# Performance work log

Measured on AMD Instinct MI355X. Metric: run time of the kernel, lower is better.

## Reference

```python
import jax, jax.numpy as jnp
import numpy as np

N = 8192
NFEAT = 512
NHID = 512
NCLASS = 64
NLAYERS = 8
LAMDA = 0.5
ALPHA = 0.1
EDGE_P = 0.002  # ~16 avg degree


def setup_inputs() -> dict:
    key = jax.random.key(0)
    ks = jax.random.split(key, 6)
    x = jax.random.normal(ks[0], (N, NFEAT), dtype=jnp.float32)
    # sparse 0/1 adjacency, densified (the original densifies adj each layer)
    adj = (jax.random.uniform(ks[1], (N, N)) < EDGE_P).astype(jnp.float32)
    stdv1 = 1.0 / np.sqrt(NHID)
    fc1_W = jax.random.normal(ks[2], (NFEAT, NHID), dtype=jnp.float32) * stdv1
    fc1_b = jnp.zeros((NHID,), dtype=jnp.float32)
    # GraphConvolution.reset_parameters: uniform(-1/sqrt(out), 1/sqrt(out))
    conv_Ws = jax.random.uniform(ks[3], (NLAYERS, NHID, NHID), minval=-stdv1, maxval=stdv1, dtype=jnp.float32)
    stdv2 = 1.0 / np.sqrt(NCLASS)
    fc2_W = jax.random.normal(ks[4], (NHID, NCLASS), dtype=jnp.float32) * stdv2
    fc2_b = jnp.zeros((NCLASS,), dtype=jnp.float32)
    return {"x": x, "adj": adj, "fc1_W": fc1_W, "fc1_b": fc1_b,
            "conv_Ws": conv_Ws, "fc2_W": fc2_W, "fc2_b": fc2_b}


def reference(x, adj, fc1_W, fc1_b, conv_Ws, fc2_W, fc2_b):
    n = adj.shape[0]
    # A_hat = A + I ; P = D^{-1/2} A_hat D^{-1/2}  (diag matmuls -> row/col scaling)
    A_hat = adj + jnp.eye(n, dtype=adj.dtype)
    dinv = 1.0 / jnp.sqrt(jnp.sum(A_hat, axis=0))  # [N]
    P = dinv[:, None] * A_hat * dinv[None, :]      # identical every layer; compute once

    H0 = jax.nn.relu(x @ fc1_W + fc1_b)            # fc1 (dropout is identity: training=False)
    H = H0
    for i in range(NLAYERS):
        beta = float(np.log(LAMDA / (i + 1) + 1.0))
        init_res = (1.0 - ALPHA) * (P @ H) + ALPHA * H0
        # init_res @ ((1-beta) I + beta W) expanded:
        H = jax.nn.relu((1.0 - beta) * init_res + beta * (init_res @ conv_Ws[i]))
    logits = H @ fc2_W + fc2_b
    return -jax.nn.log_softmax(logits, axis=1)
```

## Files before the change

kernel.cpp:

```cpp
#include <hip/hip_runtime.h>
#include <hip/hip_bf16.h>
#include <cmath>

#define N_NODES 8192
#define NFEAT 512
#define NHID 512
#define NCLASS 64
#define NLAYERS 8
#define CAP 96

typedef __attribute__((ext_vector_type(8))) short bf16x8;
typedef __attribute__((ext_vector_type(4))) float f32x4;
typedef unsigned short u16;

__device__ inline float bf2f(short u) {
  union { unsigned int i; float f; } x;
  x.i = ((unsigned int)(u16)u) << 16;
  return x.f;
}
__device__ inline short f2bf(float f) {
  union { float f; unsigned int i; } x;
  x.f = f;
  unsigned int r = x.i + 0x7FFFu + ((x.i >> 16) & 1u);
  return (short)(r >> 16);
}

__global__ __launch_bounds__(256)
void extract_kernel(const float* __restrict__ adj, int* __restrict__ idx,
                    int* __restrict__ cnt, int* __restrict__ colcnt)
{
  __shared__ int s_cnt;
  const int i = blockIdx.x;
  if (threadIdx.x == 0) s_cnt = 0;
  __syncthreads();
  const uint4* row = (const uint4*)(adj + (size_t)i * N_NODES);
  for (int c = threadIdx.x; c < N_NODES / 4; c += 256) {
    uint4 v = row[c];
    if ((v.x | v.y | v.z | v.w) == 0u) continue;
    unsigned int vals[4] = {v.x, v.y, v.z, v.w};
    #pragma unroll
    for (int e = 0; e < 4; ++e) {
      if (vals[e] != 0u) {
        int p = atomicAdd(&s_cnt, 1);
        if (p < CAP) idx[(size_t)i * CAP + p] = c * 4 + e;
        atomicAdd(&colcnt[c * 4 + e], 1);
      }
    }
  }
  __syncthreads();
  if (threadIdx.x == 0) cnt[i] = min(s_cnt, CAP);
}

__global__ __launch_bounds__(256)
void dinv_kernel(const int* __restrict__ colcnt, float* __restrict__ dinv)
{
  int j = blockIdx.x * 256 + threadIdx.x;
  if (j < N_NODES) dinv[j] = 1.0f / sqrtf((float)colcnt[j] + 1.0f);
}

__global__ __launch_bounds__(256)
void cvt_bf16_kernel(const float* __restrict__ src, u16* __restrict__ dst, int n4)
{
  int i = blockIdx.x * 256 + threadIdx.x;
  if (i >= n4) return;
  float4 v = ((const float4*)src)[i];
  ushort4 o;
  o.x = (u16)f2bf(v.x); o.y = (u16)f2bf(v.y);
  o.z = (u16)f2bf(v.z); o.w = (u16)f2bf(v.w);
  ((ushort4*)dst)[i] = o;
}

__global__ __launch_bounds__(256)
void transpose_cast_kernel(const float* __restrict__ fc1W, const float* __restrict__ convW,
                           u16* __restrict__ Wt)
{
  __shared__ float tile[32][33];
  const int m = blockIdx.z;
  const float* src = (m == 0) ? fc1W : convW + (size_t)(m - 1) * NHID * NHID;
  u16* dst = Wt + (size_t)m * NHID * NHID;
  const int k0 = blockIdx.x * 32, n0 = blockIdx.y * 32;
  const int tx = threadIdx.x & 31, ty = threadIdx.x >> 5;
  #pragma unroll
  for (int r = 0; r < 32; r += 8)
    tile[ty + r][tx] = src[(size_t)(k0 + ty + r) * NHID + n0 + tx];
  __syncthreads();
  #pragma unroll
  for (int r = 0; r < 32; r += 8)
    dst[(size_t)(n0 + ty + r) * NHID + k0 + tx] = (u16)f2bf(tile[tx][ty + r]);
}

#define AS1 __attribute__((address_space(1)))
#define AS3 __attribute__((address_space(3)))

__device__ inline void load16(const void* g, void* l) {
  __builtin_amdgcn_global_load_lds((const AS1 void*)g, (AS3 void*)l, 16, 0, 0);
}

template<int MODE>
__global__ __launch_bounds__(256, 2)
void gemm_kernel(const u16* __restrict__ A, const u16* __restrict__ Bt,
                 const float* __restrict__ bias, const u16* __restrict__ skip,
                 const float* __restrict__ dinv, float cA, float cB,
                 u16* __restrict__ out0, u16* __restrict__ out1)
{
  constexpr int K = 512, N = 512;
  __shared__ u16 ldsA[2][64 * 32];
  __shared__ u16 ldsB[2][128 * 32];
  const int tid = threadIdx.x;
  const int wave = tid >> 6, lane = tid & 63;
  const int m0 = blockIdx.x * 64, n0 = blockIdx.y * 128;
  const int wr = wave >> 1, wc = wave & 1;
  const int lrow = lane & 15, lk = lane >> 4;

  f32x4 acc[2][4];
  #pragma unroll
  for (int a = 0; a < 2; ++a)
    #pragma unroll
    for (int b = 0; b < 4; ++b)
      acc[a][b] = (f32x4){0.f, 0.f, 0.f, 0.f};

  auto stage = [&](int b, int ks) {
    {
      const int c = wave * 64 + lane;
      load16(A + (size_t)(m0 + (c >> 2)) * K + ks + (c & 3) * 8,
             &ldsA[b][(wave * 64) * 8]);
    }
    #pragma unroll
    for (int r = 0; r < 2; ++r) {
      const int c = r * 256 + wave * 64 + lane;
      load16(Bt + (size_t)(n0 + (c >> 2)) * K + ks + (c & 3) * 8,
             &ldsB[b][(r * 256 + wave * 64) * 8]);
    }
  };

  stage(0, 0);
  __syncthreads();

  for (int t = 0; t < 16; ++t) {
    const int b = t & 1;
    if (t + 1 < 16) stage(b ^ 1, (t + 1) * 32);
    bf16x8 af[2], bfr[4];
    #pragma unroll
    for (int mi = 0; mi < 2; ++mi)
      af[mi] = *(const bf16x8*)&ldsA[b][(wr * 32 + mi * 16 + lrow) * 32 + lk * 8];
    #pragma unroll
    for (int ni = 0; ni < 4; ++ni)
      bfr[ni] = *(const bf16x8*)&ldsB[b][(wc * 64 + ni * 16 + lrow) * 32 + lk * 8];
    #pragma unroll
    for (int mi = 0; mi < 2; ++mi)
      #pragma unroll
      for (int ni = 0; ni < 4; ++ni)
        acc[mi][ni] = __builtin_amdgcn_mfma_f32_16x16x32_bf16(af[mi], bfr[ni], acc[mi][ni], 0, 0, 0);
    __syncthreads();
  }

  #pragma unroll
  for (int mi = 0; mi < 2; ++mi) {
    #pragma unroll
    for (int ni = 0; ni < 4; ++ni) {
      #pragma unroll
      for (int r = 0; r < 4; ++r) {
        const int row = m0 + wr * 32 + mi * 16 + lk * 4 + r;
        const int col = n0 + wc * 64 + ni * 16 + lrow;
        const size_t o = (size_t)row * N + col;
        float v = acc[mi][ni][r];
        if (MODE == 0) {
          v = fmaxf(v + bias[col], 0.f);
          out0[o] = (u16)f2bf(v);
          out1[o] = (u16)f2bf(dinv[row] * v);
        } else {
          v = fmaxf(cA * bf2f((short)skip[o]) + cB * v, 0.f);
          out0[o] = (u16)f2bf(MODE == 1 ? dinv[row] * v : v);
        }
      }
    }
  }
}

__global__ __launch_bounds__(256)
void spmm_kernel(const u16* __restrict__ Hs, const u16* __restrict__ H0,
                 const float* __restrict__ dinv, const int* __restrict__ idx,
                 const int* __restrict__ cnt, u16* __restrict__ IR)
{
  const int wave = threadIdx.x >> 6, lane = threadIdx.x & 63;
  const int i = blockIdx.x * 4 + wave;
  const int c0 = lane * 8;
  const int n = cnt[i];
  int jreg = 0;
  if (lane < n) jreg = idx[(size_t)i * CAP + lane] & (N_NODES - 1);

  float acc[8];
  #pragma unroll
  for (int e = 0; e < 8; ++e) acc[e] = 0.f;

  const int nn = min(n, 64);
  int t = 0;
  for (; t + 8 <= nn; t += 8) {
    bf16x8 v[8];
    #pragma unroll
    for (int u = 0; u < 8; ++u) {
      const int j = __shfl(jreg, t + u);
      v[u] = *(const bf16x8*)&Hs[(size_t)j * NHID + c0];
    }
    #pragma unroll
    for (int u = 0; u < 8; ++u)
      #pragma unroll
      for (int e = 0; e < 8; ++e)
        acc[e] += bf2f(v[u][e]);
  }
  for (; t < nn; ++t) {
    const int j = __shfl(jreg, t);
    bf16x8 v = *(const bf16x8*)&Hs[(size_t)j * NHID + c0];
    #pragma unroll
    for (int e = 0; e < 8; ++e) acc[e] += bf2f(v[e]);
  }
  for (; t < n; ++t) {
    const int j = idx[(size_t)i * CAP + t] & (N_NODES - 1);
    bf16x8 v = *(const bf16x8*)&Hs[(size_t)j * NHID + c0];
    #pragma unroll
    for (int e = 0; e < 8; ++e) acc[e] += bf2f(v[e]);
  }

  const float di = dinv[i];
  bf16x8 self = *(const bf16x8*)&Hs[(size_t)i * NHID + c0];
  bf16x8 h0   = *(const bf16x8*)&H0[(size_t)i * NHID + c0];
  bf16x8 ov;
  #pragma unroll
  for (int e = 0; e < 8; ++e) {
    float v = 0.9f * di * (acc[e] + bf2f(self[e])) + 0.1f * bf2f(h0[e]);
    ov[e] = f2bf(v);
  }
  *(bf16x8*)&IR[(size_t)i * NHID + c0] = ov;
}

__global__ __launch_bounds__(256)
void fc2_softmax_kernel(const u16* __restrict__ H, const float* __restrict__ W,
                        const float* __restrict__ b, float* __restrict__ out)
{
  __shared__ float sh[4][4][512];
  const int wave = threadIdx.x >> 6, lane = threadIdx.x & 63;
  const int rowBase = blockIdx.x * 16 + wave * 4;
  #pragma unroll
  for (int rr = 0; rr < 4; ++rr) {
    bf16x8 hv = *(const bf16x8*)&H[(size_t)(rowBase + rr) * NHID + lane * 8];
    #pragma unroll
    for (int e = 0; e < 8; ++e) sh[wave][rr][lane * 8 + e] = bf2f(hv[e]);
  }
  __syncthreads();
  const float bb = b[lane];
  float a0 = bb, a1 = bb, a2 = bb, a3 = bb;
  #pragma unroll 8
  for (int k = 0; k < 512; ++k) {
    const float w = W[k * 64 + lane];
    a0 += sh[wave][0][k] * w;
    a1 += sh[wave][1][k] * w;
    a2 += sh[wave][2][k] * w;
    a3 += sh[wave][3][k] * w;
  }
  float accs[4] = {a0, a1, a2, a3};
  #pragma unroll
  for (int rr = 0; rr < 4; ++rr) {
    const float v = accs[rr];
    float mx = v;
    for (int off = 32; off > 0; off >>= 1) mx = fmaxf(mx, __shfl_xor(mx, off));
    float s = __expf(v - mx);
    for (int off = 32; off > 0; off >>= 1) s += __shfl_xor(s, off);
    out[(size_t)(rowBase + rr) * NCLASS + lane] = -(v - mx - logf(s));
  }
}

extern "C" void kernel_launch(void* const* d_in, const int* in_sizes, int n_in,
                              void* d_out, int out_size, void* d_ws, size_t ws_size,
                              hipStream_t stream)
{
  const float* x     = (const float*)d_in[0];
  const float* adj   = (const float*)d_in[1];
  const float* fc1W  = (const float*)d_in[2];
  const float* fc1b  = (const float*)d_in[3];
  const float* convW = (const float*)d_in[4];
  const float* fc2W  = (const float*)d_in[5];
  const float* fc2b  = (const float*)d_in[6];
  float* out = (float*)d_out;

  char* ws = (char*)d_ws;
  size_t off = 0;
  auto alloc = [&](size_t bytes) -> void* {
    void* p = ws + off;
    off = (off + bytes + 255) & ~(size_t)255;
    return p;
  };
  u16*   xb   = (u16*)alloc((size_t)N_NODES * NFEAT * 2);
  u16*   Wt   = (u16*)alloc((size_t)9 * NHID * NHID * 2);
  u16*   H0   = (u16*)alloc((size_t)N_NODES * NHID * 2);
  u16*   HsA  = (u16*)alloc((size_t)N_NODES * NHID * 2);
  u16*   HsB  = (u16*)alloc((size_t)N_NODES * NHID * 2);
  u16*   IR   = (u16*)alloc((size_t)N_NODES * NHID * 2);
  int*   idx  = (int*)alloc((size_t)N_NODES * CAP * 4);
  int*   cnt  = (int*)alloc((size_t)N_NODES * 4);
  int*   colc = (int*)alloc((size_t)N_NODES * 4);
  float* dinv = (float*)alloc((size_t)N_NODES * 4);

  hipMemsetAsync(colc, 0, N_NODES * 4, stream);
  extract_kernel<<<N_NODES, 256, 0, stream>>>(adj, idx, cnt, colc);
  dinv_kernel<<<N_NODES / 256, 256, 0, stream>>>(colc, dinv);
  cvt_bf16_kernel<<<(N_NODES * NFEAT / 4) / 256, 256, 0, stream>>>(x, xb, N_NODES * NFEAT / 4);
  transpose_cast_kernel<<<dim3(16, 16, 9), 256, 0, stream>>>(fc1W, convW, Wt);

  gemm_kernel<0><<<dim3(128, 4), 256, 0, stream>>>(xb, Wt, fc1b, nullptr, dinv, 0.f, 0.f, H0, HsA);

  const u16* Hin = HsA;
  for (int i = 0; i < NLAYERS; ++i) {
    const double beta = log(0.5 / (double)(i + 1) + 1.0);
    const float cA = (float)(1.0 - beta), cB = (float)beta;
    spmm_kernel<<<N_NODES / 4, 256, 0, stream>>>(Hin, H0, dinv, idx, cnt, IR);
    u16* Hout = (Hin == HsA) ? HsB : HsA;
    if (i < NLAYERS - 1)
      gemm_kernel<1><<<dim3(128, 4), 256, 0, stream>>>(
          IR, Wt + (size_t)(i + 1) * NHID * NHID, nullptr, IR, dinv, cA, cB, Hout, nullptr);
    else
      gemm_kernel<2><<<dim3(128, 4), 256, 0, stream>>>(
          IR, Wt + (size_t)(i + 1) * NHID * NHID, nullptr, IR, dinv, cA, cB, Hout, nullptr);
    Hin = Hout;
  }

  fc2_softmax_kernel<<<N_NODES / 16, 256, 0, stream>>>((const u16*)Hin, fc2W, fc2b, out);
}
```

Baseline: 361.8 us.

## Fuse all post-extract stages into one persistent kernel with grid barriers

Result: slower. 1.155 ms (+219.3%).

```diff
diff --git a/kernel.cpp b/kernel.cpp
--- a/kernel.cpp
+++ b/kernel.cpp
@@ -8,10 +8,13 @@
 #define NCLASS 64
 #define NLAYERS 8
 #define CAP 96
+#define NBLK 512
 
 typedef __attribute__((ext_vector_type(8))) short bf16x8;
 typedef __attribute__((ext_vector_type(4))) float f32x4;
 typedef unsigned short u16;
+
+struct Coefs { float cA[8]; float cB[8]; };
 
 __device__ inline float bf2f(short u) {
   union { unsigned int i; float f; } x;
@@ -51,42 +54,69 @@
   if (threadIdx.x == 0) cnt[i] = min(s_cnt, CAP);
 }
 
-__global__ __launch_bounds__(256)
-void dinv_kernel(const int* __restrict__ colcnt, float* __restrict__ dinv)
-{
-  int j = blockIdx.x * 256 + threadIdx.x;
-  if (j < N_NODES) dinv[j] = 1.0f / sqrtf((float)colcnt[j] + 1.0f);
-}
-
-__global__ __launch_bounds__(256)
-void cvt_bf16_kernel(const float* __restrict__ src, u16* __restrict__ dst, int n4)
-{
-  int i = blockIdx.x * 256 + threadIdx.x;
-  if (i >= n4) return;
-  float4 v = ((const float4*)src)[i];
-  ushort4 o;
-  o.x = (u16)f2bf(v.x); o.y = (u16)f2bf(v.y);
-  o.z = (u16)f2bf(v.z); o.w = (u16)f2bf(v.w);
-  ((ushort4*)dst)[i] = o;
-}
-
-__global__ __launch_bounds__(256)
-void transpose_cast_kernel(const float* __restrict__ fc1W, const float* __restrict__ convW,
-                           u16* __restrict__ Wt)
-{
-  __shared__ float tile[32][33];
-  const int m = blockIdx.z;
-  const float* src = (m == 0) ? fc1W : convW + (size_t)(m - 1) * NHID * NHID;
-  u16* dst = Wt + (size_t)m * NHID * NHID;
-  const int k0 = blockIdx.x * 32, n0 = blockIdx.y * 32;
+__device__ inline void gridbar(int* bar, int phase) {
+  __syncthreads();
+  if (threadIdx.x == 0) {
+    __hip_atomic_fetch_add(&bar[phase], 1, __ATOMIC_RELEASE, __HIP_MEMORY_SCOPE_AGENT);
+    while (__hip_atomic_load(&bar[phase], __ATOMIC_RELAXED, __HIP_MEMORY_SCOPE_AGENT) < NBLK)
+      __builtin_amdgcn_s_sleep(1);
+    __builtin_amdgcn_fence(__ATOMIC_ACQUIRE, "agent");
+  }
+  __syncthreads();
+}
+
+__device__ void p_dinv(const int* __restrict__ colc, float* __restrict__ dinv) {
+  if (blockIdx.x < N_NODES / 256) {
+    const int j = blockIdx.x * 256 + threadIdx.x;
+    dinv[j] = 1.0f / sqrtf((float)colc[j] + 1.0f);
+  }
+}
+
+__device__ void p_cvt(const float* __restrict__ x, u16* __restrict__ xb) {
+  const float4* src = (const float4*)x;
+  #pragma unroll
+  for (int it = 0; it < 8; ++it) {
+    const int i = it * (NBLK * 256) + blockIdx.x * 256 + threadIdx.x;
+    float4 v = src[i];
+    ushort4 o;
+    o.x = (u16)f2bf(v.x); o.y = (u16)f2bf(v.y);
+    o.z = (u16)f2bf(v.z); o.w = (u16)f2bf(v.w);
+    ((ushort4*)xb)[i] = o;
+  }
+}
+
+__device__ void p_transpose(const float* __restrict__ fc1W, const float* __restrict__ convW,
+                            u16* __restrict__ Wt, const Coefs& co, char* smem) {
+  float (*tile)[33] = (float(*)[33])smem;
   const int tx = threadIdx.x & 31, ty = threadIdx.x >> 5;
-  #pragma unroll
-  for (int r = 0; r < 32; r += 8)
-    tile[ty + r][tx] = src[(size_t)(k0 + ty + r) * NHID + n0 + tx];
-  __syncthreads();
-  #pragma unroll
-  for (int r = 0; r < 32; r += 8)
-    dst[(size_t)(n0 + ty + r) * NHID + k0 + tx] = (u16)f2bf(tile[tx][ty + r]);
+  for (int it = 0; it < 5; ++it) {
+    const int vb = it * NBLK + blockIdx.x;
+    const bool valid = vb < 2304;
+    int m = 0, k0 = 0, n0 = 0;
+    const float* src = nullptr;
+    u16* dst = nullptr;
+    float cA = 0.f, cB = 1.f;
+    if (valid) {
+      m = vb >> 8; k0 = (vb & 15) * 32; n0 = ((vb >> 4) & 15) * 32;
+      src = (m == 0) ? fc1W : convW + (size_t)(m - 1) * NHID * NHID;
+      dst = Wt + (size_t)m * NHID * NHID;
+      if (m >= 1) { cA = co.cA[m - 1]; cB = co.cB[m - 1]; }
+      #pragma unroll
+      for (int r = 0; r < 32; r += 8)
+        tile[ty + r][tx] = src[(size_t)(k0 + ty + r) * NHID + n0 + tx];
+    }
+    __syncthreads();
+    if (valid) {
+      #pragma unroll
+      for (int r = 0; r < 32; r += 8) {
+        const int krow = k0 + tx, ncol = n0 + ty + r;
+        float val = cB * tile[tx][ty + r];
+        if (m >= 1 && krow == ncol) val += cA;
+        dst[(size_t)ncol * NHID + krow] = (u16)f2bf(val);
+      }
+    }
+    __syncthreads();
+  }
 }
 
 #define AS1 __attribute__((address_space(1)))
@@ -96,148 +126,160 @@
   __builtin_amdgcn_global_load_lds((const AS1 void*)g, (AS3 void*)l, 16, 0, 0);
 }
 
-template<int MODE>
-__global__ __launch_bounds__(256, 2)
-void gemm_kernel(const u16* __restrict__ A, const u16* __restrict__ Bt,
-                 const float* __restrict__ bias, const u16* __restrict__ skip,
-                 const float* __restrict__ dinv, float cA, float cB,
-                 u16* __restrict__ out0, u16* __restrict__ out1)
+__device__ void gemm_phase(const u16* __restrict__ A, const u16* __restrict__ Bt,
+                           const float* __restrict__ bias, const float* __restrict__ dinv,
+                           u16* __restrict__ out0, u16* __restrict__ out1,
+                           int mode, char* smem)
 {
   constexpr int K = 512, N = 512;
-  __shared__ u16 ldsA[2][64 * 32];
-  __shared__ u16 ldsB[2][128 * 32];
+  u16* ldsA = (u16*)smem;
+  u16* ldsB = (u16*)(smem + 16384);
   const int tid = threadIdx.x;
   const int wave = tid >> 6, lane = tid & 63;
-  const int m0 = blockIdx.x * 64, n0 = blockIdx.y * 128;
-  const int wr = wave >> 1, wc = wave & 1;
+  const int m0 = (blockIdx.x & 127) * 64;
+  const int n0 = (blockIdx.x >> 7) * 128;
   const int lrow = lane & 15, lk = lane >> 4;
 
-  f32x4 acc[2][4];
-  #pragma unroll
-  for (int a = 0; a < 2; ++a)
-    #pragma unroll
-    for (int b = 0; b < 4; ++b)
+  f32x4 acc[4][2];
+  #pragma unroll
+  for (int a = 0; a < 4; ++a)
+    #pragma unroll
+    for (int b = 0; b < 2; ++b)
       acc[a][b] = (f32x4){0.f, 0.f, 0.f, 0.f};
 
   auto stage = [&](int b, int ks) {
-    {
-      const int c = wave * 64 + lane;
-      load16(A + (size_t)(m0 + (c >> 2)) * K + ks + (c & 3) * 8,
-             &ldsA[b][(wave * 64) * 8]);
-    }
     #pragma unroll
     for (int r = 0; r < 2; ++r) {
       const int c = r * 256 + wave * 64 + lane;
-      load16(Bt + (size_t)(n0 + (c >> 2)) * K + ks + (c & 3) * 8,
-             &ldsB[b][(r * 256 + wave * 64) * 8]);
+      const int row = c >> 3, sc = (c & 7) ^ (row & 7);
+      load16(A + (size_t)(m0 + row) * K + ks + sc * 8,
+             &ldsA[b * 4096 + (r * 256 + wave * 64) * 8]);
+    }
+    #pragma unroll
+    for (int r = 0; r < 4; ++r) {
+      const int c = r * 256 + wave * 64 + lane;
+      const int row = c >> 3, sc = (c & 7) ^ (row & 7);
+      load16(Bt + (size_t)(n0 + row) * K + ks + sc * 8,
+             &ldsB[b * 8192 + (r * 256 + wave * 64) * 8]);
     }
   };
 
   stage(0, 0);
   __syncthreads();
 
-  for (int t = 0; t < 16; ++t) {
+  for (int t = 0; t < K / 64; ++t) {
     const int b = t & 1;
-    if (t + 1 < 16) stage(b ^ 1, (t + 1) * 32);
-    bf16x8 af[2], bfr[4];
-    #pragma unroll
-    for (int mi = 0; mi < 2; ++mi)
-      af[mi] = *(const bf16x8*)&ldsA[b][(wr * 32 + mi * 16 + lrow) * 32 + lk * 8];
-    #pragma unroll
-    for (int ni = 0; ni < 4; ++ni)
-      bfr[ni] = *(const bf16x8*)&ldsB[b][(wc * 64 + ni * 16 + lrow) * 32 + lk * 8];
-    #pragma unroll
-    for (int mi = 0; mi < 2; ++mi)
-      #pragma unroll
-      for (int ni = 0; ni < 4; ++ni)
-        acc[mi][ni] = __builtin_amdgcn_mfma_f32_16x16x32_bf16(af[mi], bfr[ni], acc[mi][ni], 0, 0, 0);
+    if (t + 1 < K / 64) stage(b ^ 1, (t + 1) * 64);
+    const char* pA = (const char*)(ldsA + b * 4096);
+    const char* pB = (const char*)(ldsB + b * 8192);
+    #pragma unroll
+    for (int ks2 = 0; ks2 < 2; ++ks2) {
+      const int j = ks2 * 4 + lk;
+      bf16x8 af[4], bfr[2];
+      #pragma unroll
+      for (int mi = 0; mi < 4; ++mi) {
+        const int row = mi * 16 + lrow;
+        af[mi] = *(const bf16x8*)(pA + row * 128 + ((j ^ (row & 7)) * 16));
+      }
+      #pragma unroll
+      for (int ni = 0; ni < 2; ++ni) {
+        const int row = wave * 32 + ni * 16 + lrow;
+        bfr[ni] = *(const bf16x8*)(pB + row * 128 + ((j ^ (row & 7)) * 16));
+      }
+      #pragma unroll
+      for (int mi = 0; mi < 4; ++mi)
+        #pragma unroll
+        for (int ni = 0; ni < 2; ++ni)
+          acc[mi][ni] = __builtin_amdgcn_mfma_f32_16x16x32_bf16(af[mi], bfr[ni], acc[mi][ni], 0, 0, 0);
+    }
     __syncthreads();
   }
 
   #pragma unroll
-  for (int mi = 0; mi < 2; ++mi) {
-    #pragma unroll
-    for (int ni = 0; ni < 4; ++ni) {
+  for (int mi = 0; mi < 4; ++mi) {
+    #pragma unroll
+    for (int ni = 0; ni < 2; ++ni) {
       #pragma unroll
       for (int r = 0; r < 4; ++r) {
-        const int row = m0 + wr * 32 + mi * 16 + lk * 4 + r;
-        const int col = n0 + wc * 64 + ni * 16 + lrow;
+        const int row = m0 + mi * 16 + lk * 4 + r;
+        const int col = n0 + wave * 32 + ni * 16 + lrow;
         const size_t o = (size_t)row * N + col;
         float v = acc[mi][ni][r];
-        if (MODE == 0) {
+        if (mode == 0) {
           v = fmaxf(v + bias[col], 0.f);
           out0[o] = (u16)f2bf(v);
           out1[o] = (u16)f2bf(dinv[row] * v);
         } else {
-          v = fmaxf(cA * bf2f((short)skip[o]) + cB * v, 0.f);
-          out0[o] = (u16)f2bf(MODE == 1 ? dinv[row] * v : v);
+          v = fmaxf(v, 0.f);
+          out0[o] = (u16)f2bf(mode == 1 ? dinv[row] * v : v);
         }
       }
     }
   }
 }
 
-__global__ __launch_bounds__(256)
-void spmm_kernel(const u16* __restrict__ Hs, const u16* __restrict__ H0,
-                 const float* __restrict__ dinv, const int* __restrict__ idx,
-                 const int* __restrict__ cnt, u16* __restrict__ IR)
+__device__ void spmm_phase(const u16* __restrict__ Hs, const u16* __restrict__ H0,
+                           const float* __restrict__ dinv, const int* __restrict__ idx,
+                           const int* __restrict__ cnt, u16* __restrict__ IR)
 {
   const int wave = threadIdx.x >> 6, lane = threadIdx.x & 63;
-  const int i = blockIdx.x * 4 + wave;
+  const int xcd = blockIdx.x & 7, q = blockIdx.x >> 3;
+  const int p = xcd + 8 * (q >> 2);
+  const int row0 = p * 64 + (q & 3) * 16 + wave * 4;
   const int c0 = lane * 8;
-  const int n = cnt[i];
-  int jreg = 0;
-  if (lane < n) jreg = idx[(size_t)i * CAP + lane] & (N_NODES - 1);
-
-  float acc[8];
-  #pragma unroll
-  for (int e = 0; e < 8; ++e) acc[e] = 0.f;
-
-  const int nn = min(n, 64);
-  int t = 0;
-  for (; t + 8 <= nn; t += 8) {
-    bf16x8 v[8];
-    #pragma unroll
-    for (int u = 0; u < 8; ++u) {
-      const int j = __shfl(jreg, t + u);
-      v[u] = *(const bf16x8*)&Hs[(size_t)j * NHID + c0];
-    }
-    #pragma unroll
-    for (int u = 0; u < 8; ++u)
-      #pragma unroll
-      for (int e = 0; e < 8; ++e)
-        acc[e] += bf2f(v[u][e]);
-  }
-  for (; t < nn; ++t) {
-    const int j = __shfl(jreg, t);
-    bf16x8 v = *(const bf16x8*)&Hs[(size_t)j * NHID + c0];
-    #pragma unroll
-    for (int e = 0; e < 8; ++e) acc[e] += bf2f(v[e]);
-  }
-  for (; t < n; ++t) {
-    const int j = idx[(size_t)i * CAP + t] & (N_NODES - 1);
-    bf16x8 v = *(const bf16x8*)&Hs[(size_t)j * NHID + c0];
-    #pragma unroll
-    for (int e = 0; e < 8; ++e) acc[e] += bf2f(v[e]);
-  }
-
-  const float di = dinv[i];
-  bf16x8 self = *(const bf16x8*)&Hs[(size_t)i * NHID + c0];
-  bf16x8 h0   = *(const bf16x8*)&H0[(size_t)i * NHID + c0];
-  bf16x8 ov;
-  #pragma unroll
-  for (int e = 0; e < 8; ++e) {
-    float v = 0.9f * di * (acc[e] + bf2f(self[e])) + 0.1f * bf2f(h0[e]);
-    ov[e] = f2bf(v);
-  }
-  *(bf16x8*)&IR[(size_t)i * NHID + c0] = ov;
-}
-
-__global__ __launch_bounds__(256)
-void fc2_softmax_kernel(const u16* __restrict__ H, const float* __restrict__ W,
-                        const float* __restrict__ b, float* __restrict__ out)
-{
-  __shared__ float sh[4][4][512];
+  for (int rr = 0; rr < 4; ++rr) {
+    const int i = row0 + rr;
+    const int n = cnt[i];
+    int jreg = 0;
+    if (lane < n) jreg = idx[(size_t)i * CAP + lane] & (N_NODES - 1);
+    float acc[8];
+    #pragma unroll
+    for (int e = 0; e < 8; ++e) acc[e] = 0.f;
+    const int nn = min(n, 64);
+    int t = 0;
+    for (; t + 8 <= nn; t += 8) {
+      bf16x8 v[8];
+      #pragma unroll
+      for (int u = 0; u < 8; ++u) {
+        const int j = __shfl(jreg, t + u);
+        v[u] = *(const bf16x8*)&Hs[(size_t)j * NHID + c0];
+      }
+      #pragma unroll
+      for (int u = 0; u < 8; ++u)
+        #pragma unroll
+        for (int e = 0; e < 8; ++e)
+          acc[e] += bf2f(v[u][e]);
+    }
+    for (; t < nn; ++t) {
+      const int j = __shfl(jreg, t);
+      bf16x8 v = *(const bf16x8*)&Hs[(size_t)j * NHID + c0];
+      #pragma unroll
+      for (int e = 0; e < 8; ++e) acc[e] += bf2f(v[e]);
+    }
+    for (; t < n; ++t) {
+      const int j = idx[(size_t)i * CAP + t] & (N_NODES - 1);
+      bf16x8 v = *(const bf16x8*)&Hs[(size_t)j * NHID + c0];
+      #pragma unroll
+      for (int e = 0; e < 8; ++e) acc[e] += bf2f(v[e]);
+    }
+    const float di = dinv[i];
+    bf16x8 self = *(const bf16x8*)&Hs[(size_t)i * NHID + c0];
+    bf16x8 h0   = *(const bf16x8*)&H0[(size_t)i * NHID + c0];
+    bf16x8 ov;
+    #pragma unroll
+    for (int e = 0; e < 8; ++e) {
+      float v = 0.9f * di * (acc[e] + bf2f(self[e])) + 0.1f * bf2f(h0[e]);
+      ov[e] = f2bf(v);
+    }
+    *(bf16x8*)&IR[(size_t)i * NHID + c0] = ov;
+  }
+}
+
+__device__ void fc2_phase(const u16* __restrict__ H, const float* __restrict__ W,
+                          const float* __restrict__ b, float* __restrict__ out,
+                          char* smem)
+{
+  float (*sh)[4][512] = (float(*)[4][512])smem;
   const int wave = threadIdx.x >> 6, lane = threadIdx.x & 63;
   const int rowBase = blockIdx.x * 16 + wave * 4;
   #pragma unroll
@@ -262,11 +304,48 @@
   for (int rr = 0; rr < 4; ++rr) {
     const float v = accs[rr];
     float mx = v;
+    #pragma unroll
     for (int off = 32; off > 0; off >>= 1) mx = fmaxf(mx, __shfl_xor(mx, off));
     float s = __expf(v - mx);
+    #pragma unroll
     for (int off = 32; off > 0; off >>= 1) s += __shfl_xor(s, off);
     out[(size_t)(rowBase + rr) * NCLASS + lane] = -(v - mx - logf(s));
   }
+}
+
+__global__ __launch_bounds__(256, 2)
+void mega_kernel(const float* __restrict__ x, const float* __restrict__ fc1W,
+                 const float* __restrict__ fc1b, const float* __restrict__ convW,
+                 const float* __restrict__ fc2W, const float* __restrict__ fc2b,
+                 const int* __restrict__ colc, const int* __restrict__ idx,
+                 const int* __restrict__ cnt,
+                 u16* __restrict__ xb, u16* __restrict__ Wt, float* __restrict__ dinv,
+                 u16* __restrict__ H0, u16* __restrict__ HsA, u16* __restrict__ HsB,
+                 u16* __restrict__ IR, float* __restrict__ out,
+                 int* __restrict__ bar, Coefs co)
+{
+  __shared__ char smem[49152];
+
+  p_dinv(colc, dinv);
+  p_cvt(x, xb);
+  p_transpose(fc1W, convW, Wt, co, smem);
+  gridbar(bar, 0);
+
+  gemm_phase(xb, Wt, fc1b, dinv, H0, HsA, 0, smem);
+  gridbar(bar, 1);
+
+  const u16* Hin = HsA;
+  for (int l = 0; l < NLAYERS; ++l) {
+    spmm_phase(Hin, H0, dinv, idx, cnt, IR);
+    gridbar(bar, 2 + 2 * l);
+    u16* Hout = (l & 1) ? HsA : HsB;
+    gemm_phase(IR, Wt + (size_t)(l + 1) * NHID * NHID, nullptr, dinv,
+               Hout, nullptr, (l < NLAYERS - 1) ? 1 : 2, smem);
+    gridbar(bar, 3 + 2 * l);
+    Hin = Hout;
+  }
+
+  fc2_phase(Hin, fc2W, fc2b, out, smem);
 }
 
 extern "C" void kernel_launch(void* const* d_in, const int* in_sizes, int n_in,
@@ -297,31 +376,20 @@
   u16*   IR   = (u16*)alloc((size_t)N_NODES * NHID * 2);
   int*   idx  = (int*)alloc((size_t)N_NODES * CAP * 4);
   int*   cnt  = (int*)alloc((size_t)N_NODES * 4);
+  float* dinv = (float*)alloc((size_t)N_NODES * 4);
   int*   colc = (int*)alloc((size_t)N_NODES * 4);
-  float* dinv = (float*)alloc((size_t)N_NODES * 4);
-
-  hipMemsetAsync(colc, 0, N_NODES * 4, stream);
-  extract_kernel<<<N_NODES, 256, 0, stream>>>(adj, idx, cnt, colc);
-  dinv_kernel<<<N_NODES / 256, 256, 0, stream>>>(colc, dinv);
-  cvt_bf16_kernel<<<(N_NODES * NFEAT / 4) / 256, 256, 0, stream>>>(x, xb, N_NODES * NFEAT / 4);
-  transpose_cast_kernel<<<dim3(16, 16, 9), 256, 0, stream>>>(fc1W, convW, Wt);
-
-  gemm_kernel<0><<<dim3(128, 4), 256, 0, stream>>>(xb, Wt, fc1b, nullptr, dinv, 0.f, 0.f, H0, HsA);
-
-  const u16* Hin = HsA;
+  int*   bar  = (int*)alloc(128);
+
+  Coefs co;
   for (int i = 0; i < NLAYERS; ++i) {
     const double beta = log(0.5 / (double)(i + 1) + 1.0);
-    const float cA = (float)(1.0 - beta), cB = (float)beta;
-    spmm_kernel<<<N_NODES / 4, 256, 0, stream>>>(Hin, H0, dinv, idx, cnt, IR);
-    u16* Hout = (Hin == HsA) ? HsB : HsA;
-    if (i < NLAYERS - 1)
-      gemm_kernel<1><<<dim3(128, 4), 256, 0, stream>>>(
-          IR, Wt + (size_t)(i + 1) * NHID * NHID, nullptr, IR, dinv, cA, cB, Hout, nullptr);
-    else
-      gemm_kernel<2><<<dim3(128, 4), 256, 0, stream>>>(
-          IR, Wt + (size_t)(i + 1) * NHID * NHID, nullptr, IR, dinv, cA, cB, Hout, nullptr);
-    Hin = Hout;
-  }
-
-  fc2_softmax_kernel<<<N_NODES / 16, 256, 0, stream>>>((const u16*)Hin, fc2W, fc2b, out);
-}
+    co.cA[i] = (float)(1.0 - beta);
+    co.cB[i] = (float)beta;
+  }
+
+  hipMemsetAsync(colc, 0, (size_t)N_NODES * 4 + 128, stream);
+  extract_kernel<<<N_NODES, 256, 0, stream>>>(adj, idx, cnt, colc);
+  mega_kernel<<<NBLK, 256, 0, stream>>>(x, fc1W, fc1b, convW, fc2W, fc2b,
+                                        colc, idx, cnt, xb, Wt, dinv,
+                                        H0, HsA, HsB, IR, out, bar, co);
+}
```
